# Kernel optimization log

Measured on AMD Instinct MI355X. Metric: run time of the kernel, lower is better.

## Reference

```python
import jax, jax.numpy as jnp
import numpy as np

NUM_HEADS = 32

def setup_inputs() -> dict:
    key = jax.random.key(0)
    k1, k2, k3 = jax.random.split(key, 3)
    B, C, H, W = 4, 768, 32, 32
    x = jax.random.normal(k1, (B, C, H, W), dtype=jnp.float32)
    # 1x1 conv kernels represented as [C_in, C_out] matrices
    w_qkv = jax.random.normal(k2, (C, 3 * C), dtype=jnp.float32) * (2.0 / (3 * C)) ** 0.5
    b_qkv = jnp.zeros((3 * C,), dtype=jnp.float32)
    w_proj = jax.random.normal(k3, (C, C), dtype=jnp.float32) * (2.0 / C) ** 0.5
    b_proj = jnp.zeros((C,), dtype=jnp.float32)
    return {"x": x, "w_qkv": w_qkv, "b_qkv": b_qkv, "w_proj": w_proj, "b_proj": b_proj}

def reference(x, w_qkv, b_qkv, w_proj, b_proj):
    B, C, H, W = x.shape
    h = NUM_HEADS
    hd = C // h
    scale = hd ** (-0.5)
    # qkv 1x1 conv (channels_first): [B,C,H,W] -> [B,3C,H,W]
    qkv = jnp.einsum('bchw,cd->bdhw', x, w_qkv) + b_qkv[None, :, None, None]
    qkv = qkv.reshape(B, 3, h, hd, H * W)
    q = qkv[:, 0]  # [B,h,hd,HW]
    k = qkv[:, 1]  # [B,h,hd,HW]
    v = qkv[:, 2]  # [B,h,hd,HW]
    # attn = q^T @ k : [B,h,HW,HW]
    attn = jnp.einsum('bhdq,bhdk->bhqk', q, k) * scale
    attn = jax.nn.softmax(attn, axis=-1)
    # out = (attn @ v^T)^T : [B,h,hd,HW]
    o = jnp.einsum('bhqk,bhdk->bhdq', attn, v)
    o = o.reshape(B, C, H, W)
    # proj 1x1 conv
    out = jnp.einsum('bchw,cf->bfhw', o, w_proj) + b_proj[None, :, None, None]
    return out
```

## Files before the change

kernel.cpp:

```cpp
#include <hip/hip_runtime.h>
#include <hip/hip_bf16.h>

#define B_  4
#define C_  768
#define N_  1024
#define NH  32
#define HD  24
#define HDP 32
#define D3  2304
#define QSCALE 0.29448889f

typedef __hip_bfloat16 bf16;
typedef __attribute__((ext_vector_type(8))) short bf16x8;
typedef __attribute__((ext_vector_type(4))) float f32x4;

__device__ __forceinline__ unsigned cvt_pk_bf16(float lo, float hi) {
    unsigned r;
    asm volatile("v_cvt_pk_bf16_f32 %0, %1, %2" : "=v"(r) : "v"(lo), "v"(hi));
    return r;
}

__device__ __forceinline__ float fast_exp2(float x) {
    float r;
    asm volatile("v_exp_f32 %0, %1" : "=v"(r) : "v"(x));
    return r;
}

__global__ __launch_bounds__(256) void prep(
        const float* __restrict__ x, const float* __restrict__ w_qkv,
        const float* __restrict__ w_proj,
        bf16* __restrict__ xt, bf16* __restrict__ wqT, bf16* __restrict__ wpT,
        bf16* __restrict__ vB) {
    const int bid = blockIdx.x;
    if (bid >= 5376) {
        const int head = bid - 5376;
        bf16* row = vB + ((size_t)head * HDP + 24) * N_;
        const ushort4 ones = {0x3F80, 0x3F80, 0x3F80, 0x3F80};
        *(ushort4*)&row[threadIdx.x * 4] = ones;
        return;
    }
    const float* src; bf16* dst; int R, Cc, r0, c0;
    if (bid < 3072) {
        const int b = bid / 768, rem = bid % 768;
        R = 768; Cc = 1024;
        src = x + (size_t)b * 768 * 1024;
        dst = xt + (size_t)b * 1024 * 768;
        c0 = (rem % 32) * 32; r0 = (rem / 32) * 32;
    } else if (bid < 4800) {
        const int rem = bid - 3072;
        R = 768; Cc = 2304; src = w_qkv; dst = wqT;
        c0 = (rem % 72) * 32; r0 = (rem / 72) * 32;
    } else {
        const int rem = bid - 4800;
        R = 768; Cc = 768; src = w_proj; dst = wpT;
        c0 = (rem % 24) * 32; r0 = (rem / 24) * 32;
    }
    __shared__ float tile[32][33];
    const int tx = threadIdx.x & 31, ty = threadIdx.x >> 5;
    #pragma unroll
    for (int k = 0; k < 4; k++)
        tile[ty + 8*k][tx] = src[(size_t)(r0 + ty + 8*k) * Cc + c0 + tx];
    __syncthreads();
    #pragma unroll
    for (int k = 0; k < 4; k++)
        dst[(size_t)(c0 + ty + 8*k) * R + r0 + tx] = __float2bfloat16(tile[tx][ty + 8*k]);
}

__global__ __launch_bounds__(256) void gemm_qkv(
        const bf16* __restrict__ xt, const bf16* __restrict__ wqT,
        const float* __restrict__ bqkv,
        bf16* __restrict__ qT, bf16* __restrict__ kT, bf16* __restrict__ vB) {
    __shared__ bf16 As[2][64 * 32];
    __shared__ bf16 Bs[2][128 * 32];

    const int bid0 = blockIdx.x;
    const int bid = (bid0 & 7) * 144 + (bid0 >> 3);
    const bool vmode = (bid >= 768);
    const bf16* Ap; const bf16* Bp; int M0, Nc0;
    if (!vmode) {
        Ap = xt;                       Bp = wqT;
        M0 = (bid & 63) * 64;          Nc0 = (bid >> 6) * 128;
    } else {
        const int r = bid - 768;
        Ap = wqT + (size_t)1536 * C_;  Bp = xt;
        M0 = (r % 12) * 64;            Nc0 = (r / 12) * 128;
    }

    const int t = threadIdx.x;
    const int lane = t & 63, wid = t >> 6;
    const int c = lane & 15, g = lane >> 4;
    const int wm = wid >> 1, wn = wid & 1;

    const int srow = t >> 2, schunk = (t & 3) * 8;
    const bf16* Ag  = Ap + (size_t)(M0 + srow) * C_ + schunk;
    const bf16* Bga = Bp + (size_t)(Nc0 + srow) * C_ + schunk;
    const bf16* Bgb = Bga + (size_t)64 * C_;
    const int aws = srow * 32 + schunk;
    const int bws = srow * 32 + schunk;

    f32x4 acc[2][4];
    #pragma unroll
    for (int i = 0; i < 2; i++)
        #pragma unroll
        for (int j = 0; j < 4; j++) acc[i][j] = f32x4{0.f, 0.f, 0.f, 0.f};

    int4 ra  = *(const int4*)Ag;
    int4 rb0 = *(const int4*)Bga;
    int4 rb1 = *(const int4*)Bgb;
    *(int4*)&As[0][aws] = ra;
    *(int4*)&Bs[0][bws] = rb0;
    *(int4*)&Bs[0][bws + 64 * 32] = rb1;
    ra  = *(const int4*)(Ag + 32);
    rb0 = *(const int4*)(Bga + 32);
    rb1 = *(const int4*)(Bgb + 32);
    __syncthreads();

    #pragma unroll 2
    for (int s = 0; s < 24; s++) {
        const int cb = s & 1;
        bf16x8 af[2], bfr[4];
        #pragma unroll
        for (int mi = 0; mi < 2; mi++)
            af[mi] = *(const bf16x8*)&As[cb][(wm * 32 + mi * 16 + c) * 32 + g * 8];
        #pragma unroll
        for (int ni = 0; ni < 4; ni++)
            bfr[ni] = *(const bf16x8*)&Bs[cb][(wn * 64 + ni * 16 + c) * 32 + g * 8];
        __builtin_amdgcn_s_setprio(1);
        #pragma unroll
        for (int mi = 0; mi < 2; mi++)
            #pragma unroll
            for (int ni = 0; ni < 4; ni++)
                acc[mi][ni] = __builtin_amdgcn_mfma_f32_16x16x32_bf16(
                    af[mi], bfr[ni], acc[mi][ni], 0, 0, 0);
        __builtin_amdgcn_s_setprio(0);
        if (s < 23) {
            __syncthreads();
            *(int4*)&As[cb ^ 1][aws] = ra;
            *(int4*)&Bs[cb ^ 1][bws] = rb0;
            *(int4*)&Bs[cb ^ 1][bws + 64 * 32] = rb1;
            if (s < 22) {
                const int k1 = (s + 2) * 32;
                ra  = *(const int4*)(Ag + k1);
                rb0 = *(const int4*)(Bga + k1);
                rb1 = *(const int4*)(Bgb + k1);
            }
            __syncthreads();
        }
    }

    const int row0 = M0 + wm * 32, col0 = Nc0 + wn * 64;
    if (!vmode) {
        #pragma unroll
        for (int ni = 0; ni < 4; ni++) {
            const int j = col0 + ni * 16 + c;
            const int issec = j >= 768;
            bf16* dstbase = issec ? kT : qT;
            const int dd = j - (issec ? 768 : 0);
            const int hh = dd / 24, hd = dd % 24;
            const float bq = bqkv[j];
            const float sca = issec ? 1.0f : QSCALE;
            #pragma unroll
            for (int mi = 0; mi < 2; mi++)
                #pragma unroll
                for (int r = 0; r < 4; r++) {
                    const int n = row0 + mi * 16 + 4 * g + r;
                    const int b = n >> 10, nn = n & 1023;
                    dstbase[(((size_t)(b * NH + hh) * N_) + nn) * HDP + hd] =
                        __float2bfloat16((acc[mi][ni][r] + bq) * sca);
                }
        }
    } else {
        #pragma unroll
        for (int mi = 0; mi < 2; mi++)
            #pragma unroll
            for (int r = 0; r < 4; r++) {
                const int vd = row0 + mi * 16 + 4 * g + r;
                const int hh = vd / 24, hd = vd % 24;
                const float bq = bqkv[1536 + vd];
                #pragma unroll
                for (int ni = 0; ni < 4; ni++) {
                    const int n = col0 + ni * 16 + c;
                    const int b = n >> 10, nn = n & 1023;
                    vB[((size_t)(b * NH + hh) * HDP + hd) * N_ + nn] =
                        __float2bfloat16(acc[mi][ni][r] + bq);
                }
            }
    }
}

__global__ __launch_bounds__(256) void gemm_proj(
        const bf16* __restrict__ wpT, const bf16* __restrict__ obuf,
        const float* __restrict__ bproj, float* __restrict__ outF) {
    __shared__ bf16 As[2][64 * 32];
    __shared__ bf16 Bs[2][128 * 32];

    const int bid0 = blockIdx.x;
    const int bid = (bid0 & 7) * 48 + (bid0 >> 3);
    const int mt = bid % 12, rem = bid / 12;
    const int nt = rem & 7, b = rem >> 3;
    const bf16* Ap = wpT;
    const bf16* Bp = obuf + (size_t)b * N_ * C_;
    const int M0 = mt * 64, Nc0 = nt * 128;

    const int t = threadIdx.x;
    const int lane = t & 63, wid = t >> 6;
    const int c = lane & 15, g = lane >> 4;
    const int wm = wid >> 1, wn = wid & 1;

    const int srow = t >> 2, schunk = (t & 3) * 8;
    const bf16* Ag  = Ap + (size_t)(M0 + srow) * C_ + schunk;
    const bf16* Bga = Bp + (size_t)(Nc0 + srow) * C_ + schunk;
    const bf16* Bgb = Bga + (size_t)64 * C_;
    const int aws = srow * 32 + schunk;
    const int bws = srow * 32 + schunk;

    f32x4 acc[2][4];
    #pragma unroll
    for (int i = 0; i < 2; i++)
        #pragma unroll
        for (int j = 0; j < 4; j++) acc[i][j] = f32x4{0.f, 0.f, 0.f, 0.f};

    int4 ra  = *(const int4*)Ag;
    int4 rb0 = *(const int4*)Bga;
    int4 rb1 = *(const int4*)Bgb;
    *(int4*)&As[0][aws] = ra;
    *(int4*)&Bs[0][bws] = rb0;
    *(int4*)&Bs[0][bws + 64 * 32] = rb1;
    ra  = *(const int4*)(Ag + 32);
    rb0 = *(const int4*)(Bga + 32);
    rb1 = *(const int4*)(Bgb + 32);
    __syncthreads();

    #pragma unroll 2
    for (int s = 0; s < 24; s++) {
        const int cb = s & 1;
        bf16x8 af[2], bfr[4];
        #pragma unroll
        for (int mi = 0; mi < 2; mi++)
            af[mi] = *(const bf16x8*)&As[cb][(wm * 32 + mi * 16 + c) * 32 + g * 8];
        #pragma unroll
        for (int ni = 0; ni < 4; ni++)
            bfr[ni] = *(const bf16x8*)&Bs[cb][(wn * 64 + ni * 16 + c) * 32 + g * 8];
        __builtin_amdgcn_s_setprio(1);
        #pragma unroll
        for (int mi = 0; mi < 2; mi++)
            #pragma unroll
            for (int ni = 0; ni < 4; ni++)
                acc[mi][ni] = __builtin_amdgcn_mfma_f32_16x16x32_bf16(
                    af[mi], bfr[ni], acc[mi][ni], 0, 0, 0);
        __builtin_amdgcn_s_setprio(0);
        if (s < 23) {
            __syncthreads();
            *(int4*)&As[cb ^ 1][aws] = ra;
            *(int4*)&Bs[cb ^ 1][bws] = rb0;
            *(int4*)&Bs[cb ^ 1][bws + 64 * 32] = rb1;
            if (s < 22) {
                const int k1 = (s + 2) * 32;
                ra  = *(const int4*)(Ag + k1);
                rb0 = *(const int4*)(Bga + k1);
                rb1 = *(const int4*)(Bgb + k1);
            }
            __syncthreads();
        }
    }

    const int row0 = M0 + wm * 32, col0 = Nc0 + wn * 64;
    #pragma unroll
    for (int mi = 0; mi < 2; mi++)
        #pragma unroll
        for (int r = 0; r < 4; r++) {
            const int f = row0 + mi * 16 + 4 * g + r;
            const float bp = bproj[f];
            #pragma unroll
            for (int ni = 0; ni < 4; ni++) {
                const int n = col0 + ni * 16 + c;
                outF[((size_t)b * C_ + f) * N_ + n] = acc[mi][ni][r] + bp;
            }
        }
}

__global__ __launch_bounds__(256) void attn_mfma(
        const bf16* __restrict__ qT, const bf16* __restrict__ kT,
        const bf16* __restrict__ vB, bf16* __restrict__ obuf) {
    __shared__ bf16 Kb[2][64 * 40];
    __shared__ bf16 Vb[2][32 * 72];
    __shared__ bf16 Ps[4][32 * 72];

    const int t = threadIdx.x, lane = t & 63, wid = t >> 6;
    const int c = lane & 15, g = lane >> 4;
    const int bid = blockIdx.x;
    const int xcd = bid & 7, idx = bid >> 3;
    const int hl = xcd * 16 + (idx & 15);
    const int qb = idx >> 4;
    const int b = hl >> 5, h = hl & 31;
    const int q0 = qb * 128 + wid * 32;
    const size_t hb = (size_t)(b * NH + h);
    const bf16* qh = qT + hb * N_ * HDP;
    const bf16* kh = kT + hb * N_ * HDP;
    const bf16* vh = vB + hb * HDP * N_;
    bf16* myPs = &Ps[wid][0];

    bf16x8 qf0 = *(const bf16x8*)(qh + (size_t)(q0 + c) * HDP + g * 8);
    bf16x8 qf1 = *(const bf16x8*)(qh + (size_t)(q0 + 16 + c) * HDP + g * 8);
    if (g == 3) {
        const bf16x8 z8 = {0, 0, 0, 0, 0, 0, 0, 0};
        qf0 = z8; qf1 = z8;
    }
    f32x4 o00 = {0.f,0.f,0.f,0.f}, o01 = {0.f,0.f,0.f,0.f};
    f32x4 o10 = {0.f,0.f,0.f,0.f}, o11 = {0.f,0.f,0.f,0.f};

    const bf16* kgp = kh + (size_t)(t >> 2) * HDP + (t & 3) * 8;
    const bf16* vgp = vh + (size_t)(t >> 3) * N_ + (t & 7) * 8;
    const int kws = (t >> 2) * 40 + (t & 3) * 8;
    const int vws = (t >> 3) * 72 + (t & 7) * 8;

    int4 rk = *(const int4*)kgp;
    int4 rv = *(const int4*)vgp;
    *(int4*)&Kb[0][kws] = rk;
    *(int4*)&Vb[0][vws] = rv;
    __syncthreads();

    int cur = 0;
    for (int kt = 0; kt < 16; kt++) {
        if (kt < 15) {
            const int k1 = (kt + 1) * 64;
            rk = *(const int4*)(kgp + (size_t)k1 * HDP);
            rv = *(const int4*)(vgp + k1);
        }
        f32x4 st0[4], st1[4];
        __builtin_amdgcn_s_setprio(1);
        #pragma unroll
        for (int tt = 0; tt < 4; tt++) {
            bf16x8 kf = *(const bf16x8*)&Kb[cur][(tt * 16 + c) * 40 + g * 8];
            f32x4 z = {0.f, 0.f, 0.f, 0.f};
            st0[tt] = __builtin_amdgcn_mfma_f32_16x16x32_bf16(kf, qf0, z, 0, 0, 0);
            st1[tt] = __builtin_amdgcn_mfma_f32_16x16x32_bf16(kf, qf1, z, 0, 0, 0);
        }
        __builtin_amdgcn_s_setprio(0);
        float p0[16], p1[16];
        #pragma unroll
        for (int tt = 0; tt < 4; tt++)
            #pragma unroll
            for (int r = 0; r < 4; r++) {
                p0[tt * 4 + r] = fast_exp2(st0[tt][r]);
                p1[tt * 4 + r] = fast_exp2(st1[tt][r]);
            }
        #pragma unroll
        for (int tt = 0; tt < 4; tt++) {
            uint2 w0, w1;
            w0.x = cvt_pk_bf16(p0[tt * 4 + 0], p0[tt * 4 + 1]);
            w0.y = cvt_pk_bf16(p0[tt * 4 + 2], p0[tt * 4 + 3]);
            w1.x = cvt_pk_bf16(p1[tt * 4 + 0], p1[tt * 4 + 1]);
            w1.y = cvt_pk_bf16(p1[tt * 4 + 2], p1[tt * 4 + 3]);
            *(uint2*)&myPs[c * 72 + tt * 16 + g * 4]        = w0;
            *(uint2*)&myPs[(16 + c) * 72 + tt * 16 + g * 4] = w1;
        }
        bf16x8 pa00 = *(const bf16x8*)&myPs[c * 72 + g * 8];
        bf16x8 pa01 = *(const bf16x8*)&myPs[c * 72 + 32 + g * 8];
        bf16x8 pa10 = *(const bf16x8*)&myPs[(16 + c) * 72 + g * 8];
        bf16x8 pa11 = *(const bf16x8*)&myPs[(16 + c) * 72 + 32 + g * 8];

        bf16x8 va0 = *(const bf16x8*)&Vb[cur][c * 72 + g * 8];
        bf16x8 va1 = *(const bf16x8*)&Vb[cur][c * 72 + 32 + g * 8];
        bf16x8 vb0 = *(const bf16x8*)&Vb[cur][(16 + c) * 72 + g * 8];
        bf16x8 vb1 = *(const bf16x8*)&Vb[cur][(16 + c) * 72 + 32 + g * 8];
        __builtin_amdgcn_s_setprio(1);
        o00 = __builtin_amdgcn_mfma_f32_16x16x32_bf16(pa00, va0, o00, 0, 0, 0);
        o00 = __builtin_amdgcn_mfma_f32_16x16x32_bf16(pa01, va1, o00, 0, 0, 0);
        o01 = __builtin_amdgcn_mfma_f32_16x16x32_bf16(pa00, vb0, o01, 0, 0, 0);
        o01 = __builtin_amdgcn_mfma_f32_16x16x32_bf16(pa01, vb1, o01, 0, 0, 0);
        o10 = __builtin_amdgcn_mfma_f32_16x16x32_bf16(pa10, va0, o10, 0, 0, 0);
        o10 = __builtin_amdgcn_mfma_f32_16x16x32_bf16(pa11, va1, o10, 0, 0, 0);
        o11 = __builtin_amdgcn_mfma_f32_16x16x32_bf16(pa10, vb0, o11, 0, 0, 0);
        o11 = __builtin_amdgcn_mfma_f32_16x16x32_bf16(pa11, vb1, o11, 0, 0, 0);
        __builtin_amdgcn_s_setprio(0);

        if (kt < 15) {
            *(int4*)&Kb[cur ^ 1][kws] = rk;
            *(int4*)&Vb[cur ^ 1][vws] = rv;
        }
        __syncthreads();
        cur ^= 1;
    }

    float inv0[4], inv1[4];
    #pragma unroll
    for (int r = 0; r < 4; r++) {
        inv0[r] = 1.f / __shfl(o01[r], g * 16 + 8);
        inv1[r] = 1.f / __shfl(o11[r], g * 16 + 8);
    }
    #pragma unroll
    for (int dt = 0; dt < 2; dt++) {
        const int dcol = dt * 16 + c;
        if (dcol < HD) {
            const f32x4 oa = dt ? o01 : o00;
            const f32x4 ob = dt ? o11 : o10;
            #pragma unroll
            for (int r = 0; r < 4; r++) {
                const int qa = q0 + g * 4 + r;
                const int qb2 = q0 + 16 + g * 4 + r;
                obuf[((size_t)b * N_ + qa) * C_ + h * HD + dcol] =
                    __float2bfloat16(oa[r] * inv0[r]);
                obuf[((size_t)b * N_ + qb2) * C_ + h * HD + dcol] =
                    __float2bfloat16(ob[r] * inv1[r]);
            }
        }
    }
}

extern "C" void kernel_launch(void* const* d_in, const int* in_sizes, int n_in,
                              void* d_out, int out_size, void* d_ws, size_t ws_size,
                              hipStream_t stream) {
    const float* x      = (const float*)d_in[0];
    const float* w_qkv  = (const float*)d_in[1];
    const float* b_qkv  = (const float*)d_in[2];
    const float* w_proj = (const float*)d_in[3];
    const float* b_proj = (const float*)d_in[4];
    float* out = (float*)d_out;

    char* ws = (char*)d_ws;
    bf16* xt   = (bf16*)(ws);
    bf16* wqT  = (bf16*)(ws + 6291456);
    bf16* wpT  = (bf16*)(ws + 9830400);
    bf16* qT   = (bf16*)(ws + 11010048);
    bf16* kT   = (bf16*)(ws + 19398656);
    bf16* vB   = (bf16*)(ws + 27787264);
    bf16* obuf = (bf16*)(ws + 36175872);

    prep<<<dim3(5504), 256, 0, stream>>>(x, w_qkv, w_proj, xt, wqT, wpT, vB);
    gemm_qkv<<<dim3(1152), 256, 0, stream>>>(xt, wqT, b_qkv, qT, kT, vB);
    attn_mfma<<<dim3(1024), 256, 0, stream>>>(qT, kT, vB, obuf);
    gemm_proj<<<dim3(384), 256, 0, stream>>>(wpT, obuf, b_proj, out);
}
```

Measured before the change: 156.4 us.

## Enlarge QKV GEMM tiles, swizzle LDS layout, deepen global prefetch

```diff
diff --git a/kernel.cpp b/kernel.cpp
--- a/kernel.cpp
+++ b/kernel.cpp
@@ -70,64 +70,66 @@
         const bf16* __restrict__ xt, const bf16* __restrict__ wqT,
         const float* __restrict__ bqkv,
         bf16* __restrict__ qT, bf16* __restrict__ kT, bf16* __restrict__ vB) {
-    __shared__ bf16 As[2][64 * 32];
+    __shared__ bf16 As[2][128 * 32];
     __shared__ bf16 Bs[2][128 * 32];
 
     const int bid0 = blockIdx.x;
-    const int bid = (bid0 & 7) * 144 + (bid0 >> 3);
-    const bool vmode = (bid >= 768);
+    const int bid = (bid0 & 7) * 72 + (bid0 >> 3);
+    const bool vmode = (bid >= 384);
     const bf16* Ap; const bf16* Bp; int M0, Nc0;
     if (!vmode) {
         Ap = xt;                       Bp = wqT;
-        M0 = (bid & 63) * 64;          Nc0 = (bid >> 6) * 128;
+        M0 = (bid & 31) * 128;         Nc0 = (bid >> 5) * 128;
     } else {
-        const int r = bid - 768;
+        const int r = bid - 384;
         Ap = wqT + (size_t)1536 * C_;  Bp = xt;
-        M0 = (r % 12) * 64;            Nc0 = (r / 12) * 128;
+        M0 = (r % 6) * 128;            Nc0 = (r / 6) * 128;
     }
 
     const int t = threadIdx.x;
     const int lane = t & 63, wid = t >> 6;
     const int c = lane & 15, g = lane >> 4;
     const int wm = wid >> 1, wn = wid & 1;
-
-    const int srow = t >> 2, schunk = (t & 3) * 8;
-    const bf16* Ag  = Ap + (size_t)(M0 + srow) * C_ + schunk;
-    const bf16* Bga = Bp + (size_t)(Nc0 + srow) * C_ + schunk;
-    const bf16* Bgb = Bga + (size_t)64 * C_;
-    const int aws = srow * 32 + schunk;
-    const int bws = srow * 32 + schunk;
-
-    f32x4 acc[2][4];
-    #pragma unroll
-    for (int i = 0; i < 2; i++)
+    const int sg = (g ^ ((c >> 1) & 3)) * 8;
+
+    const int srow = t >> 2;
+    const int swc = ((t & 3) ^ ((srow >> 1) & 3)) * 8;
+    const bf16* Ag0 = Ap + (size_t)(M0 + srow) * C_ + (t & 3) * 8;
+    const bf16* Ag1 = Ag0 + (size_t)64 * C_;
+    const bf16* Bg0 = Bp + (size_t)(Nc0 + srow) * C_ + (t & 3) * 8;
+    const bf16* Bg1 = Bg0 + (size_t)64 * C_;
+    const int w0 = srow * 32 + swc, w1 = (srow + 64) * 32 + swc;
+
+    f32x4 acc[4][4];
+    #pragma unroll
+    for (int i = 0; i < 4; i++)
         #pragma unroll
         for (int j = 0; j < 4; j++) acc[i][j] = f32x4{0.f, 0.f, 0.f, 0.f};
 
-    int4 ra  = *(const int4*)Ag;
-    int4 rb0 = *(const int4*)Bga;
-    int4 rb1 = *(const int4*)Bgb;
-    *(int4*)&As[0][aws] = ra;
-    *(int4*)&Bs[0][bws] = rb0;
-    *(int4*)&Bs[0][bws + 64 * 32] = rb1;
-    ra  = *(const int4*)(Ag + 32);
-    rb0 = *(const int4*)(Bga + 32);
-    rb1 = *(const int4*)(Bgb + 32);
+    int4 a0A, a1A, b0A, b1A, a0B, a1B, b0B, b1B;
+    a0A = *(const int4*)Ag0;  a1A = *(const int4*)Ag1;
+    b0A = *(const int4*)Bg0;  b1A = *(const int4*)Bg1;
+    *(int4*)&As[0][w0] = a0A; *(int4*)&As[0][w1] = a1A;
+    *(int4*)&Bs[0][w0] = b0A; *(int4*)&Bs[0][w1] = b1A;
+    a0A = *(const int4*)(Ag0 + 32); a1A = *(const int4*)(Ag1 + 32);
+    b0A = *(const int4*)(Bg0 + 32); b1A = *(const int4*)(Bg1 + 32);
+    a0B = *(const int4*)(Ag0 + 64); a1B = *(const int4*)(Ag1 + 64);
+    b0B = *(const int4*)(Bg0 + 64); b1B = *(const int4*)(Bg1 + 64);
     __syncthreads();
 
     #pragma unroll 2
     for (int s = 0; s < 24; s++) {
         const int cb = s & 1;
-        bf16x8 af[2], bfr[4];
-        #pragma unroll
-        for (int mi = 0; mi < 2; mi++)
-            af[mi] = *(const bf16x8*)&As[cb][(wm * 32 + mi * 16 + c) * 32 + g * 8];
+        bf16x8 af[4], bfr[4];
+        #pragma unroll
+        for (int mi = 0; mi < 4; mi++)
+            af[mi] = *(const bf16x8*)&As[cb][(wm * 64 + mi * 16 + c) * 32 + sg];
         #pragma unroll
         for (int ni = 0; ni < 4; ni++)
-            bfr[ni] = *(const bf16x8*)&Bs[cb][(wn * 64 + ni * 16 + c) * 32 + g * 8];
+            bfr[ni] = *(const bf16x8*)&Bs[cb][(wn * 64 + ni * 16 + c) * 32 + sg];
         __builtin_amdgcn_s_setprio(1);
         #pragma unroll
-        for (int mi = 0; mi < 2; mi++)
+        for (int mi = 0; mi < 4; mi++)
             #pragma unroll
             for (int ni = 0; ni < 4; ni++)
                 acc[mi][ni] = __builtin_amdgcn_mfma_f32_16x16x32_bf16(
@@ -135,20 +137,28 @@
         __builtin_amdgcn_s_setprio(0);
         if (s < 23) {
             __syncthreads();
-            *(int4*)&As[cb ^ 1][aws] = ra;
-            *(int4*)&Bs[cb ^ 1][bws] = rb0;
-            *(int4*)&Bs[cb ^ 1][bws + 64 * 32] = rb1;
-            if (s < 22) {
-                const int k1 = (s + 2) * 32;
-                ra  = *(const int4*)(Ag + k1);
-                rb0 = *(const int4*)(Bga + k1);
-                rb1 = *(const int4*)(Bgb + k1);
+            if ((s & 1) == 0) {
+                *(int4*)&As[cb ^ 1][w0] = a0A; *(int4*)&As[cb ^ 1][w1] = a1A;
+                *(int4*)&Bs[cb ^ 1][w0] = b0A; *(int4*)&Bs[cb ^ 1][w1] = b1A;
+                if (s < 21) {
+                    const int k1 = (s + 3) * 32;
+                    a0A = *(const int4*)(Ag0 + k1); a1A = *(const int4*)(Ag1 + k1);
+                    b0A = *(const int4*)(Bg0 + k1); b1A = *(const int4*)(Bg1 + k1);
+                }
+            } else {
+                *(int4*)&As[cb ^ 1][w0] = a0B; *(int4*)&As[cb ^ 1][w1] = a1B;
+                *(int4*)&Bs[cb ^ 1][w0] = b0B; *(int4*)&Bs[cb ^ 1][w1] = b1B;
+                if (s < 21) {
+                    const int k1 = (s + 3) * 32;
+                    a0B = *(const int4*)(Ag0 + k1); a1B = *(const int4*)(Ag1 + k1);
+                    b0B = *(const int4*)(Bg0 + k1); b1B = *(const int4*)(Bg1 + k1);
+                }
             }
             __syncthreads();
         }
     }
 
-    const int row0 = M0 + wm * 32, col0 = Nc0 + wn * 64;
+    const int row0 = M0 + wm * 64, col0 = Nc0 + wn * 64;
     if (!vmode) {
         #pragma unroll
         for (int ni = 0; ni < 4; ni++) {
@@ -160,7 +170,7 @@
             const float bq = bqkv[j];
             const float sca = issec ? 1.0f : QSCALE;
             #pragma unroll
-            for (int mi = 0; mi < 2; mi++)
+            for (int mi = 0; mi < 4; mi++)
                 #pragma unroll
                 for (int r = 0; r < 4; r++) {
                     const int n = row0 + mi * 16 + 4 * g + r;
@@ -171,7 +181,7 @@
         }
     } else {
         #pragma unroll
-        for (int mi = 0; mi < 2; mi++)
+        for (int mi = 0; mi < 4; mi++)
             #pragma unroll
             for (int r = 0; r < 4; r++) {
                 const int vd = row0 + mi * 16 + 4 * g + r;
@@ -206,13 +216,14 @@
     const int lane = t & 63, wid = t >> 6;
     const int c = lane & 15, g = lane >> 4;
     const int wm = wid >> 1, wn = wid & 1;
-
-    const int srow = t >> 2, schunk = (t & 3) * 8;
-    const bf16* Ag  = Ap + (size_t)(M0 + srow) * C_ + schunk;
-    const bf16* Bga = Bp + (size_t)(Nc0 + srow) * C_ + schunk;
-    const bf16* Bgb = Bga + (size_t)64 * C_;
-    const int aws = srow * 32 + schunk;
-    const int bws = srow * 32 + schunk;
+    const int sg = (g ^ ((c >> 1) & 3)) * 8;
+
+    const int srow = t >> 2;
+    const int swc = ((t & 3) ^ ((srow >> 1) & 3)) * 8;
+    const bf16* Ag  = Ap + (size_t)(M0 + srow) * C_ + (t & 3) * 8;
+    const bf16* Bg0 = Bp + (size_t)(Nc0 + srow) * C_ + (t & 3) * 8;
+    const bf16* Bg1 = Bg0 + (size_t)64 * C_;
+    const int w0 = srow * 32 + swc, w1 = (srow + 64) * 32 + swc;
 
     f32x4 acc[2][4];
     #pragma unroll
@@ -220,15 +231,15 @@
         #pragma unroll
         for (int j = 0; j < 4; j++) acc[i][j] = f32x4{0.f, 0.f, 0.f, 0.f};
 
-    int4 ra  = *(const int4*)Ag;
-    int4 rb0 = *(const int4*)Bga;
-    int4 rb1 = *(const int4*)Bgb;
-    *(int4*)&As[0][aws] = ra;
-    *(int4*)&Bs[0][bws] = rb0;
-    *(int4*)&Bs[0][bws + 64 * 32] = rb1;
-    ra  = *(const int4*)(Ag + 32);
-    rb0 = *(const int4*)(Bga + 32);
-    rb1 = *(const int4*)(Bgb + 32);
+    int4 aA, b0A, b1A, aB, b0B, b1B;
+    aA  = *(const int4*)Ag;
+    b0A = *(const int4*)Bg0;  b1A = *(const int4*)Bg1;
+    *(int4*)&As[0][w0] = aA;
+    *(int4*)&Bs[0][w0] = b0A; *(int4*)&Bs[0][w1] = b1A;
+    aA  = *(const int4*)(Ag + 32);
+    b0A = *(const int4*)(Bg0 + 32); b1A = *(const int4*)(Bg1 + 32);
+    aB  = *(const int4*)(Ag + 64);
+    b0B = *(const int4*)(Bg0 + 64); b1B = *(const int4*)(Bg1 + 64);
     __syncthreads();
 
     #pragma unroll 2
@@ -237,10 +248,10 @@
         bf16x8 af[2], bfr[4];
         #pragma unroll
         for (int mi = 0; mi < 2; mi++)
-            af[mi] = *(const bf16x8*)&As[cb][(wm * 32 + mi * 16 + c) * 32 + g * 8];
+            af[mi] = *(const bf16x8*)&As[cb][(wm * 32 + mi * 16 + c) * 32 + sg];
         #pragma unroll
         for (int ni = 0; ni < 4; ni++)
-            bfr[ni] = *(const bf16x8*)&Bs[cb][(wn * 64 + ni * 16 + c) * 32 + g * 8];
+            bfr[ni] = *(const bf16x8*)&Bs[cb][(wn * 64 + ni * 16 + c) * 32 + sg];
         __builtin_amdgcn_s_setprio(1);
         #pragma unroll
         for (int mi = 0; mi < 2; mi++)
@@ -251,14 +262,22 @@
         __builtin_amdgcn_s_setprio(0);
         if (s < 23) {
             __syncthreads();
-            *(int4*)&As[cb ^ 1][aws] = ra;
-            *(int4*)&Bs[cb ^ 1][bws] = rb0;
-            *(int4*)&Bs[cb ^ 1][bws + 64 * 32] = rb1;
-            if (s < 22) {
-                const int k1 = (s + 2) * 32;
-                ra  = *(const int4*)(Ag + k1);
-                rb0 = *(const int4*)(Bga + k1);
-                rb1 = *(const int4*)(Bgb + k1);
+            if ((s & 1) == 0) {
+                *(int4*)&As[cb ^ 1][w0] = aA;
+                *(int4*)&Bs[cb ^ 1][w0] = b0A; *(int4*)&Bs[cb ^ 1][w1] = b1A;
+                if (s < 21) {
+                    const int k1 = (s + 3) * 32;
+                    aA  = *(const int4*)(Ag + k1);
+                    b0A = *(const int4*)(Bg0 + k1); b1A = *(const int4*)(Bg1 + k1);
+                }
+            } else {
+                *(int4*)&As[cb ^ 1][w0] = aB;
+                *(int4*)&Bs[cb ^ 1][w0] = b0B; *(int4*)&Bs[cb ^ 1][w1] = b1B;
+                if (s < 21) {
+                    const int k1 = (s + 3) * 32;
+                    aB  = *(const int4*)(Ag + k1);
+                    b0B = *(const int4*)(Bg0 + k1); b1B = *(const int4*)(Bg1 + k1);
+                }
             }
             __syncthreads();
         }
@@ -428,7 +447,7 @@
     bf16* obuf = (bf16*)(ws + 36175872);
 
     prep<<<dim3(5504), 256, 0, stream>>>(x, w_qkv, w_proj, xt, wqT, wpT, vB);
-    gemm_qkv<<<dim3(1152), 256, 0, stream>>>(xt, wqT, b_qkv, qT, kT, vB);
+    gemm_qkv<<<dim3(576), 256, 0, stream>>>(xt, wqT, b_qkv, qT, kT, vB);
     attn_mfma<<<dim3(1024), 256, 0, stream>>>(qT, kT, vB, obuf);
     gemm_proj<<<dim3(384), 256, 0, stream>>>(wpT, obuf, b_proj, out);
 }
```

Result: no change. 153.4 us (-1.9%).
